# Optimization experiments

Measured on AMD Instinct MI355X. Metric: run time of the kernel, lower is better.

The kernel has to match this reference:

```python
import jax, jax.numpy as jnp
import numpy as np

B, T, DIM, H, HD = 2, 2048, 1024, 8, 128
ATTN_SCALE = 0.12  # attn_args.attn_scale (modded-nanogpt constant)
F32_EPS = float(np.finfo(np.float32).eps)  # F.rms_norm default eps


def ste_round(x):
    # straight-through round (round_grad_pt): identity gradient
    return x + jax.lax.stop_gradient(jnp.round(x) - x)


def quantized_linear(x, num_bits=8, eps=1e-5):
    num_steps = (2 ** num_bits - 1) // 2  # 127
    xnmin = jnp.minimum(jnp.min(x, -1, keepdims=True), -eps)
    xpmax = jnp.maximum(jnp.max(x, -1, keepdims=True), eps)
    xp = ste_round(x / xpmax * num_steps) / num_steps * xpmax
    xn = ste_round(x / xnmin * num_steps) / num_steps * xnmin
    return jnp.where(x >= 0, xp, xn)


def ternary_quantize_mean_special(w):
    # w: [3, hdim, dim]; per-leading-slice scale
    s = jnp.maximum(jnp.mean(jnp.mean(jnp.abs(w), -1, keepdims=True), -2, keepdims=True), 1e-5)
    return s * jnp.clip(ste_round(w / s), -1.0, 1.0)


def ternary_quantize(w):
    s = jnp.maximum(jnp.mean(jnp.abs(w)), 1e-5)
    return s * jnp.clip(ste_round(w / s), -1.0, 1.0)


def rmsnorm(x):
    return x * jax.lax.rsqrt(jnp.mean(x * x, -1, keepdims=True) + F32_EPS)


def rotary(x, cos, sin):
    # x: [B,T,H,HD]; cos,sin: [T, HD//2]
    x1, x2 = jnp.split(x, 2, axis=-1)
    c = cos[None, :, None, :]
    s = sin[None, :, None, :]
    return jnp.concatenate([x1 * c + x2 * s, -x1 * s + x2 * c], axis=-1)


def setup_inputs() -> dict:
    key = jax.random.key(0)
    ks = jax.random.split(key, 5)
    x = jax.random.normal(ks[0], (B, T, DIM), jnp.float32)
    ve = jax.random.normal(ks[1], (B, T, DIM), jnp.float32)
    sa_lambdas = jnp.array([0.5, 0.5], jnp.float32)
    inv_freq = 1.0 / (10000.0 ** (np.arange(0, HD, 2, dtype=np.float32) / HD))
    ang = np.arange(T, dtype=np.float32)[:, None] * inv_freq[None, :]
    cos = jnp.asarray(np.cos(ang), jnp.float32)
    sin = jnp.asarray(np.sin(ang), jnp.float32)
    bound = (3.0 ** 0.5) * 0.5 * DIM ** (-0.5)
    qkvo_w = jax.random.uniform(ks[2], (4, H * HD, DIM), jnp.float32, -bound, bound)
    gate_w = 0.1 * jax.random.normal(ks[3], (H, 12), jnp.float32)
    return {"x": x, "ve": ve, "sa_lambdas": sa_lambdas, "cos": cos, "sin": sin,
            "qkvo_w": qkvo_w, "gate_w": gate_w}


def reference(x, ve, sa_lambdas, cos, sin, qkvo_w, gate_w):
    # pre-activation int8 fake-quant (ENABLE_ATTN_PRE_ACT_QUANTIZATION)
    xq = quantized_linear(x, num_bits=8)
    # ternary-quantized QKV weights (ENABLE_ATTN_QUANTIZATION)
    w_qkv = ternary_quantize_mean_special(qkvo_w[:3]).reshape(3 * H * HD, DIM)
    qkv = jnp.einsum('btd,ed->bte', xq, w_qkv).reshape(B, T, 3 * H, HD)
    q, k, v = qkv[:, :, :H], qkv[:, :, H:2 * H], qkv[:, :, 2 * H:]
    q, k = rmsnorm(q), rmsnorm(k)
    q, k = rotary(q, cos, sin), rotary(k, cos, sin)
    v = sa_lambdas[0] * v + sa_lambdas[1] * ve.reshape(v.shape)
    # q/k int8 fake-quant (ENABLE_ATTN_ACT_QUANTIZATION)
    q = quantized_linear(q, num_bits=8)
    k = quantized_linear(k, num_bits=8)
    # causal SDPA with explicit scale
    scores = jnp.einsum('bqhd,bkhd->bhqk', q, k) * ATTN_SCALE
    mask = jnp.tril(jnp.ones((T, T), bool))
    scores = jnp.where(mask[None, None], scores, -jnp.inf)
    p = jax.nn.softmax(scores, axis=-1)
    y = jnp.einsum('bhqk,bkhd->bqhd', p, v)  # [B,T,H,HD]
    # sigmoid gate from first 12 features of (quantized) x
    gate = jax.nn.sigmoid(jnp.einsum('btf,hf->bth', xq[..., :12], gate_w))
    y = (y * gate[..., None]).reshape(B, T, H * HD)
    # ternary-quantized output projection (ENABLE_ATTN_PROJ_QUANTIZATION)
    w_o = ternary_quantize(qkvo_w[3])
    return jnp.einsum('bte,de->btd', y, w_o)
```

## Files before the change

kernel.cpp:

```cpp
#include <hip/hip_runtime.h>
#include <hip/hip_bf16.h>
#include <cstddef>
#include <cstdint>

#define B_    2
#define T_    2048
#define DIM_  1024
#define H_    8
#define HD_   128
#define BT_   (B_*T_)
#define E3_   (3*H_*HD_)
#define F32_EPS_ 1.1920929e-07f
#define QSC_  0.17312340490667562f

typedef __attribute__((ext_vector_type(8))) short bh8_t;
typedef __attribute__((ext_vector_type(4))) float f32x4_t;
typedef __attribute__((ext_vector_type(16))) float f32x16_t;
typedef __attribute__((ext_vector_type(4))) unsigned short us4_t;

__device__ inline unsigned short bf16r(float f) {
    unsigned u = __builtin_bit_cast(unsigned, f);
    u = (u + 0x7fffu + ((u >> 16) & 1u)) >> 16;
    return (unsigned short)u;
}
__device__ inline float b2f(unsigned short u) {
    return __builtin_bit_cast(float, (unsigned)u << 16);
}
__device__ inline unsigned cvtpk(float a, float b) {
    unsigned r;
    asm("v_cvt_pk_bf16_f32 %0, %1, %2" : "=v"(r) : "v"(a), "v"(b));
    return r;
}
__device__ inline void gl16(const unsigned short* g, unsigned short* l) {
    __builtin_amdgcn_global_load_lds((const __attribute__((address_space(1))) void*)g,
                                     (__attribute__((address_space(3))) void*)l, 16, 0, 0);
}

__global__ __launch_bounds__(256) void absmean1_kernel(const float* __restrict__ w, float* __restrict__ partial) {
    int blk = blockIdx.x;
    size_t off = (size_t)blk * 4096;
    __shared__ float red[256];
    int tid = threadIdx.x;
    float acc = 0.f;
    const float* p = w + off + tid*16;
    #pragma unroll
    for (int j = 0; j < 4; j++) {
        float4 v = *(const float4*)(p + j*4);
        acc += fabsf(v.x) + fabsf(v.y) + fabsf(v.z) + fabsf(v.w);
    }
    red[tid] = acc; __syncthreads();
    for (int s = 128; s > 0; s >>= 1) { if (tid < s) red[tid] += red[tid+s]; __syncthreads(); }
    if (tid == 0) partial[blk] = red[0];
}

__global__ __launch_bounds__(256) void absmean2_kernel(const float* __restrict__ partial, float* __restrict__ scales) {
    int m = blockIdx.x;
    __shared__ float red[256];
    int tid = threadIdx.x;
    red[tid] = partial[m*256 + tid]; __syncthreads();
    for (int s = 128; s > 0; s >>= 1) { if (tid < s) red[tid] += red[tid+s]; __syncthreads(); }
    if (tid == 0) scales[m] = fmaxf(red[0] / (float)(DIM_*DIM_), 1e-5f);
}

__global__ __launch_bounds__(256) void quant_w_kernel(const float* __restrict__ w, const float* __restrict__ scales,
                                                      unsigned short* __restrict__ wq) {
    int base = (blockIdx.x * 256 + threadIdx.x) * 8;
    float s = scales[base >> 20];
    float inv = 1.f / s;
    unsigned short out[8];
    float4 v0 = *(const float4*)(w + base);
    float4 v1 = *(const float4*)(w + base + 4);
    float t[8] = {v0.x, v0.y, v0.z, v0.w, v1.x, v1.y, v1.z, v1.w};
    #pragma unroll
    for (int j = 0; j < 8; j++) {
        float r = rintf(t[j] * inv);
        r = fminf(1.f, fmaxf(-1.f, r));
        out[j] = (r == 0.f) ? 0 : (r > 0.f ? 0x3F80 : 0xBF80);
    }
    *(int4*)(wq + base) = *(const int4*)out;
}

__global__ __launch_bounds__(256) void quant_x_gate_kernel(const float* __restrict__ x, const float* __restrict__ gw,
                                                           unsigned short* __restrict__ xqb, float* __restrict__ gate) {
    int row = blockIdx.x;
    const float* xr = x + (size_t)row * DIM_;
    unsigned short* qr = xqb + (size_t)row * DIM_;
    __shared__ float red[256];
    __shared__ float x12[12];
    int tid = threadIdx.x;
    float v[4];
    float mn = 1e30f, mx = -1e30f;
    #pragma unroll
    for (int i = 0; i < 4; i++) {
        v[i] = xr[i*256 + tid];
        mn = fminf(mn, v[i]); mx = fmaxf(mx, v[i]);
    }
    red[tid] = mn; __syncthreads();
    for (int s = 128; s > 0; s >>= 1) { if (tid < s) red[tid] = fminf(red[tid], red[tid+s]); __syncthreads(); }
    mn = red[0]; __syncthreads();
    red[tid] = mx; __syncthreads();
    for (int s = 128; s > 0; s >>= 1) { if (tid < s) red[tid] = fmaxf(red[tid], red[tid+s]); __syncthreads(); }
    mx = red[0]; __syncthreads();
    float p = fmaxf(mx, 1e-5f);
    float n = fminf(mn, -1e-5f);
    #pragma unroll
    for (int i = 0; i < 4; i++) {
        int gi = i*256 + tid;
        float xv = v[i];
        float sc = (xv >= 0.f) ? p : n;
        float q = rintf(xv / sc * 127.f) / 127.f * sc;
        qr[gi] = bf16r(q);
        if (gi < 12) x12[gi] = q;
    }
    __syncthreads();
    if (tid < H_) {
        float acc = 0.f;
        #pragma unroll
        for (int f = 0; f < 12; f++) acc += x12[f] * gw[tid*12 + f];
        gate[(size_t)row * H_ + tid] = 1.f / (1.f + expf(-acc));
    }
}

template<int MT, bool OBF>
__global__ __launch_bounds__(256) void gemm_bf16_kernel(const unsigned short* __restrict__ A,
                                                        const unsigned short* __restrict__ Bm,
                                                        const float* __restrict__ sw, int sbase,
                                                        void* __restrict__ Cv, int M, int N, int K) {
    __shared__ __align__(16) unsigned short As[MT*32*64];
    __shared__ __align__(16) unsigned short Bs[128*64];
    int bm = blockIdx.y * (MT*32), bn = blockIdx.x * 128;
    int tid = threadIdx.x;
    int w = tid >> 6, l = tid & 63;
    int wr = w >> 1, wc = w & 1;
    int lg = l >> 4, lq = l & 15;
    f32x4_t acc[MT][4];
    #pragma unroll
    for (int mt = 0; mt < MT; mt++)
        #pragma unroll
        for (int nt = 0; nt < 4; nt++) acc[mt][nt] = (f32x4_t)0.f;

    for (int k0 = 0; k0 < K; k0 += 64) {
        #pragma unroll
        for (int i = 0; i < MT; i++) {
            int ob = (i*4 + w) << 10;
            int o  = ob + (l << 4);
            int row = o >> 7;
            int lcn = ((o >> 4) & 7) ^ (row & 7);
            gl16(A + (size_t)(bm+row)*K + k0 + lcn*8, (unsigned short*)As + (ob >> 1));
        }
        #pragma unroll
        for (int i = 0; i < 4; i++) {
            int ob = (i*4 + w) << 10;
            int o  = ob + (l << 4);
            int row = o >> 7;
            int lcn = ((o >> 4) & 7) ^ (row & 7);
            gl16(Bm + (size_t)(bn+row)*K + k0 + lcn*8, (unsigned short*)Bs + (ob >> 1));
        }
        __syncthreads();
        #pragma unroll
        for (int kk = 0; kk < 2; kk++) {
            bh8_t af[MT], bf[4];
            #pragma unroll
            for (int mt = 0; mt < MT; mt++) {
                int r = wr*(MT*16) + mt*16 + lq;
                int j = kk*4 + lg;
                af[mt] = *(const bh8_t*)(As + r*64 + (((j ^ (r & 7)))<<3));
            }
            #pragma unroll
            for (int nt = 0; nt < 4; nt++) {
                int r = wc*64 + nt*16 + lq;
                int j = kk*4 + lg;
                bf[nt] = *(const bh8_t*)(Bs + r*64 + (((j ^ (r & 7)))<<3));
            }
            #pragma unroll
            for (int mt = 0; mt < MT; mt++)
                #pragma unroll
                for (int nt = 0; nt < 4; nt++)
                    acc[mt][nt] = __builtin_amdgcn_mfma_f32_16x16x32_bf16(af[mt], bf[nt], acc[mt][nt], 0, 0, 0);
        }
        __syncthreads();
    }
    #pragma unroll
    for (int nt = 0; nt < 4; nt++) {
        int col = bn + wc*64 + nt*16 + lq;
        float s = sw[sbase + (col >> 10)];
        #pragma unroll
        for (int mt = 0; mt < MT; mt++) {
            int row = bm + wr*(MT*16) + mt*16 + lg*4;
            #pragma unroll
            for (int r = 0; r < 4; r++) {
                if constexpr (OBF)
                    ((unsigned short*)Cv)[(size_t)(row + r)*N + col] = bf16r(acc[mt][nt][r] * s);
                else
                    ((float*)Cv)[(size_t)(row + r)*N + col] = acc[mt][nt][r] * s;
            }
        }
    }
}

__global__ __launch_bounds__(256) void qkv_post_kernel(const unsigned short* __restrict__ qkvb,
                                                       const float* __restrict__ ve,
                                                       const float* __restrict__ lam,
                                                       const float* __restrict__ cosb, const float* __restrict__ sinb,
                                                       unsigned short* __restrict__ Qb, unsigned short* __restrict__ Kb,
                                                       unsigned short* __restrict__ Vb) {
    int bt = blockIdx.x;
    int b = bt >> 11, t = bt & (T_ - 1);
    int w = threadIdx.x >> 6, l = threadIdx.x & 63;
    const unsigned short* base = qkvb + (size_t)bt * E3_;
    float l0 = lam[0], l1 = lam[1];
    #pragma unroll
    for (int i = 0; i < 2; i++) {
        int h = w*2 + i;
        const unsigned short* row = base + (16 + h)*HD_;
        const float* ver = ve + (size_t)bt*DIM_ + h*HD_;
        unsigned short* dst = Vb + ((size_t)(b*H_+h)*T_ + t)*HD_;
        dst[l]      = bf16r(l0*b2f(row[l])    + l1*ver[l]);
        dst[l + 64] = bf16r(l0*b2f(row[l+64]) + l1*ver[l+64]);
    }
    float cc = cosb[(size_t)t*64 + l], ss = sinb[(size_t)t*64 + l];
    #pragma unroll
    for (int i = 0; i < 4; i++) {
        int part = w*4 + i;
        const unsigned short* row = base + part*HD_;
        float x1 = b2f(row[l]), x2 = b2f(row[l+64]);
        float ssq = x1*x1 + x2*x2;
        #pragma unroll
        for (int off = 1; off < 64; off <<= 1) ssq += __shfl_xor(ssq, off);
        float rms = 1.0f / sqrtf(ssq / 128.0f + F32_EPS_);
        x1 *= rms; x2 *= rms;
        float o1 = x1*cc + x2*ss;
        float o2 = -x1*ss + x2*cc;
        float mn = fminf(o1, o2), mx = fmaxf(o1, o2);
        #pragma unroll
        for (int off = 1; off < 64; off <<= 1) {
            mn = fminf(mn, __shfl_xor(mn, off));
            mx = fmaxf(mx, __shfl_xor(mx, off));
        }
        float p = fmaxf(mx, 1e-5f);
        float n = fminf(mn, -1e-5f);
        float s1 = (o1 >= 0.f) ? p : n;
        float s2 = (o2 >= 0.f) ? p : n;
        float q1 = rintf(o1 / s1 * 127.f) / 127.f * s1;
        float q2 = rintf(o2 / s2 * 127.f) / 127.f * s2;
        if (part < 8) {
            unsigned short* dst = Qb + ((size_t)(b*H_+part)*T_ + t)*HD_;
            dst[l] = bf16r(QSC_ * q1); dst[l + 64] = bf16r(QSC_ * q2);
        } else {
            unsigned short* dst = Kb + ((size_t)(b*H_+part-8)*T_ + t)*HD_;
            dst[l] = bf16r(q1); dst[l + 64] = bf16r(q2);
        }
    }
}

__global__ __launch_bounds__(256) void transpose_v_kernel(const unsigned short* __restrict__ Vb,
                                                          unsigned short* __restrict__ VT) {
    int tt = blockIdx.x;
    int dt = blockIdx.y;
    int bh = blockIdx.z;
    __shared__ unsigned short L[64][80];
    int tid = threadIdx.x;
    #pragma unroll
    for (int i = 0; i < 2; i++) {
        int c = tid + i*256;
        int r = c >> 3, dc = c & 7;
        int4 v = *(const int4*)(Vb + ((size_t)bh*T_ + tt*64 + r)*HD_ + dt*64 + dc*8);
        *(int4*)(&L[r][dc*8]) = v;
    }
    __syncthreads();
    #pragma unroll
    for (int i = 0; i < 2; i++) {
        int c = tid + i*256;
        int r = c >> 3, tc = c & 7;
        unsigned short tmp[8];
        #pragma unroll
        for (int jj = 0; jj < 8; jj++) tmp[jj] = L[tc*8+jj][r];
        *(int4*)(VT + ((size_t)bh*HD_ + dt*64 + r)*T_ + tt*64 + tc*8) = *(const int4*)tmp;
    }
}

__global__ __launch_bounds__(256) void attn_kernel(const unsigned short* __restrict__ Qb,
                                                   const unsigned short* __restrict__ Kb,
                                                   const unsigned short* __restrict__ VT,
                                                   const float* __restrict__ gate,
                                                   unsigned short* __restrict__ Yb,
                                                   unsigned short* __restrict__ Opart,
                                                   float* __restrict__ MLg) {
    __shared__ __align__(16) unsigned char SMEM[65536];
    int rid = 1279 - (int)blockIdx.x;
    int bh = rid & 15;
    int idx = rid >> 4;
    int qt, c, nc;
    if (idx < 8)       { qt = idx;                 c = 0;           nc = 1; }
    else if (idx < 24) { int t = idx - 8;  qt = 8  + (t >> 1);  c = t & 1;      nc = 2; }
    else if (idx < 48) { int t = idx - 24; qt = 16 + t / 3;     c = t - 3*(t/3); nc = 3; }
    else               { int t = idx - 48; qt = 24 + (t >> 2);  c = t & 3;      nc = 4; }
    int pslot = (idx - 8)*16 + bh;
    int b = bh >> 3, h = bh & 7;
    int tid = threadIdx.x;
    int w = tid >> 6, l = tid & 63;
    int qsub = w >> 1, qq = w & 1;
    int hh = l >> 5, l5 = l & 31;
    int qrow = qsub*32 + l5;
    int qg = qt*64 + qrow;

    const unsigned short* Kbase = Kb + (size_t)bh*T_*HD_;
    const unsigned short* Vbase = VT + (size_t)bh*HD_*T_;
    const unsigned short* Qg = Qb + ((size_t)bh*T_ + (size_t)qt*64) * HD_;

    bh8_t qf[8];
    #pragma unroll
    for (int ks = 0; ks < 8; ks++)
        qf[ks] = *(const bh8_t*)(Qg + (size_t)qrow*HD_ + ks*16 + hh*8);

    int j0c  = c*8;
    int jend = (qt + 1 < j0c + 8) ? (qt + 1) : (j0c + 8);
    int ncr  = jend - j0c;

    f32x16_t o0 = (f32x16_t)0.f, o1 = (f32x16_t)0.f, o2 = (f32x16_t)0.f, o3 = (f32x16_t)0.f;
    float mrun = -1e20f, lrun = 0.f;

#define STAGE(BI, J) { \
    unsigned short* kb_ = (unsigned short*)(SMEM + (BI)*16384); \
    unsigned short* vb_ = (unsigned short*)(SMEM + 32768 + (BI)*16384); \
    _Pragma("unroll") \
    for (int i_ = 0; i_ < 4; i_++) { \
        int ob_ = (i_*4 + w) << 10; \
        int o_  = ob_ + (l << 4); \
        int rk_ = o_ >> 8; \
        int lk_ = ((o_ >> 4) & 15) ^ (rk_ & 15); \
        gl16(Kbase + (size_t)((J)*64 + rk_)*HD_ + lk_*8, kb_ + (ob_ >> 1)); \
        int rv_ = o_ >> 7; \
        int lv_ = ((o_ >> 4) & 7) ^ (rv_ & 7); \
        gl16(Vbase + (size_t)rv_*T_ + (J)*64 + lv_*8, vb_ + (ob_ >> 1)); \
    } }

    STAGE(0, j0c);
    for (int jj = 0; jj < ncr; jj++) {
        int j = j0c + jj;
        if (jj + 1 < ncr) {
            STAGE((jj+1) & 1, j+1);
            asm volatile("s_waitcnt vmcnt(8)" ::: "memory");
        } else {
            asm volatile("s_waitcnt vmcnt(0)" ::: "memory");
        }
        __builtin_amdgcn_s_barrier();
        asm volatile("" ::: "memory");
        const unsigned short* kb = (const unsigned short*)(SMEM + (jj&1)*16384);
        const unsigned short* vb = (const unsigned short*)(SMEM + 32768 + (jj&1)*16384);
        int kvb = j*64 + qq*32;
        if (kvb <= qt*64 + qsub*32 + 31) {
            f32x16_t s = (f32x16_t)0.f;
            int krow = qq*32 + l5;
            __builtin_amdgcn_s_setprio(1);
            #pragma unroll
            for (int ks = 0; ks < 8; ks++) {
                int cch = (ks*2 + hh) ^ (krow & 15);
                bh8_t kf = *(const bh8_t*)(kb + krow*128 + cch*8);
                s = __builtin_amdgcn_mfma_f32_32x32x16_bf16(kf, qf[ks], s, 0, 0, 0);
            }
            __builtin_amdgcn_s_setprio(0);
            if (kvb + 31 > qt*64 + qsub*32) {
                #pragma unroll
                for (int r = 0; r < 16; r++) {
                    int key = kvb + (r & 3) + 8*(r >> 2) + 4*hh;
                    if (key > qg) s[r] = -1e30f;
                }
            }
            float t8[8], t4[4];
            #pragma unroll
            for (int r = 0; r < 8; r++) t8[r] = fmaxf(s[2*r], s[2*r+1]);
            #pragma unroll
            for (int r = 0; r < 4; r++) t4[r] = fmaxf(t8[2*r], t8[2*r+1]);
            float tm = fmaxf(fmaxf(t4[0], t4[1]), fmaxf(t4[2], t4[3]));
            tm = fmaxf(tm, __shfl_xor(tm, 32));
            if (!__all(tm - mrun <= 8.f)) {
                float mnew = fmaxf(mrun, tm);
                float scf = __builtin_amdgcn_exp2f(mrun - mnew);
                lrun *= scf;
                o0 *= scf; o1 *= scf; o2 *= scf; o3 *= scf;
                mrun = mnew;
            }
            float p[16];
            #pragma unroll
            for (int r = 0; r < 16; r++) p[r] = __builtin_amdgcn_exp2f(s[r] - mrun);
            #pragma unroll
            for (int r = 0; r < 8; r++) t8[r] = p[2*r] + p[2*r+1];
            #pragma unroll
            for (int r = 0; r < 4; r++) t4[r] = t8[2*r] + t8[2*r+1];
            float ls = (t4[0] + t4[1]) + (t4[2] + t4[3]);
            ls += __shfl_xor(ls, 32);
            lrun += ls;
            unsigned u0 = cvtpk(p[0], p[1]),   u1 = cvtpk(p[2], p[3]);
            unsigned u2 = cvtpk(p[4], p[5]),   u3 = cvtpk(p[6], p[7]);
            unsigned u4 = cvtpk(p[8], p[9]),   u5 = cvtpk(p[10], p[11]);
            unsigned u6 = cvtpk(p[12], p[13]), u7 = cvtpk(p[14], p[15]);
            unsigned x0 = (unsigned)__shfl_xor((int)u0, 32), x1 = (unsigned)__shfl_xor((int)u1, 32);
            unsigned x2 = (unsigned)__shfl_xor((int)u2, 32), x3 = (unsigned)__shfl_xor((int)u3, 32);
            unsigned x4 = (unsigned)__shfl_xor((int)u4, 32), x5 = (unsigned)__shfl_xor((int)u5, 32);
            unsigned x6 = (unsigned)__shfl_xor((int)u6, 32), x7 = (unsigned)__shfl_xor((int)u7, 32);
            union { bh8_t v; unsigned uu[4]; } B0, B1;
            B0.uu[0] = hh ? x2 : u0;  B0.uu[1] = hh ? x3 : u1;
            B0.uu[2] = hh ? u2 : x0;  B0.uu[3] = hh ? u3 : x1;
            B1.uu[0] = hh ? x6 : u4;  B1.uu[1] = hh ? x7 : u5;
            B1.uu[2] = hh ? u6 : x4;  B1.uu[3] = hh ? u7 : x5;
            __builtin_amdgcn_s_setprio(1);
#define PV_STEP(DT, OACC) { \
    int vrow = DT*32 + l5; \
    bh8_t vf0 = *(const bh8_t*)(vb + vrow*64 + (((qq*4 + hh) ^ (vrow & 7))<<3)); \
    OACC = __builtin_amdgcn_mfma_f32_32x32x16_bf16(vf0, B0.v, OACC, 0, 0, 0); \
    bh8_t vf1 = *(const bh8_t*)(vb + vrow*64 + (((qq*4 + 2 + hh) ^ (vrow & 7))<<3)); \
    OACC = __builtin_amdgcn_mfma_f32_32x32x16_bf16(vf1, B1.v, OACC, 0, 0, 0); }
            PV_STEP(0, o0) PV_STEP(1, o1) PV_STEP(2, o2) PV_STEP(3, o3)
#undef PV_STEP
            __builtin_amdgcn_s_setprio(0);
        }
        asm volatile("s_waitcnt lgkmcnt(0)" ::: "memory");
        __builtin_amdgcn_s_barrier();
        asm volatile("" ::: "memory");
    }

    f32x16_t oA[4] = {o0, o1, o2, o3};
    float* OB = (float*)SMEM;
    float* ML = (float*)(SMEM + 32768);
    unsigned short* YS = (unsigned short*)(SMEM + 33280);
    if (qq != 0) {
        float* obuf = OB + (size_t)qsub * 4096;
        #pragma unroll
        for (int dt = 0; dt < 4; dt++)
            #pragma unroll
            for (int g = 0; g < 4; g++) {
                f32x4_t v4;
                #pragma unroll
                for (int e = 0; e < 4; e++) v4[e] = oA[dt][g*4+e];
                int ch = (dt*4 + g) ^ (l & 7);
                *(f32x4_t*)(obuf + l*64 + ch*4) = v4;
            }
        if (hh == 0) {
            ML[(qsub*32 + l5)*2]     = mrun;
            ML[(qsub*32 + l5)*2 + 1] = lrun;
        }
    }
    __syncthreads();
    if (qq == 0) {
        float mb = ML[(qsub*32 + l5)*2];
        float lb = ML[(qsub*32 + l5)*2 + 1];
        float mN = fmaxf(mrun, mb);
        float fa = __builtin_amdgcn_exp2f(mrun - mN), fb = __builtin_amdgcn_exp2f(mb - mN);
        const float* obuf = OB + (size_t)qsub * 4096;
        #pragma unroll
        for (int dt = 0; dt < 4; dt++)
            #pragma unroll
            for (int g = 0; g < 4; g++) {
                int ch = (dt*4 + g) ^ (l & 7);
                f32x4_t v4 = *(const f32x4_t*)(obuf + l*64 + ch*4);
                #pragma unroll
                for (int e = 0; e < 4; e++)
                    oA[dt][g*4+e] = oA[dt][g*4+e]*fa + v4[e]*fb;
            }
        lrun = lrun*fa + lb*fb;
        mrun = mN;
        float inv;
        if (nc == 1) {
            float gv = gate[((size_t)b*T_ + (size_t)qg)*H_ + h];
            inv = gv / lrun;
        } else {
            inv = 1.f / lrun;
            if (hh == 0) {
                MLg[(size_t)pslot*128 + qrow*2]     = mrun;
                MLg[(size_t)pslot*128 + qrow*2 + 1] = lrun;
            }
        }
        #pragma unroll
        for (int dt = 0; dt < 4; dt++)
            #pragma unroll
            for (int g = 0; g < 4; g++) {
                unsigned short pk4[4];
                #pragma unroll
                for (int e = 0; e < 4; e++) pk4[e] = bf16r(oA[dt][g*4+e] * inv);
                int ch = (dt*4 + g) ^ (qrow & 7);
                *(us4_t*)(YS + (size_t)qrow*128 + ch*8 + hh*4) = *(const us4_t*)pk4;
            }
    }
    __syncthreads();
    if (nc == 1) {
        #pragma unroll
        for (int i = 0; i < 4; i++) {
            int idx2 = tid + i*256;
            int r = idx2 >> 4, scn = idx2 & 15;
            int lcn = scn ^ (r & 7);
            int4 v = *(const int4*)(YS + (size_t)r*128 + scn*8);
            *(int4*)(Yb + (size_t)(b*T_ + qt*64 + r)*DIM_ + h*HD_ + lcn*8) = v;
        }
    } else {
        unsigned short* od = Opart + (size_t)pslot*8192;
        #pragma unroll
        for (int i = 0; i < 4; i++) {
            int idx2 = tid + i*256;
            int r = idx2 >> 4, scn = idx2 & 15;
            int lcn = scn ^ (r & 7);
            int4 v = *(const int4*)(YS + (size_t)r*128 + scn*8);
            *(int4*)(od + (size_t)r*128 + lcn*8) = v;
        }
    }
#undef STAGE
}

__global__ __launch_bounds__(256) void attn_merge_kernel(const unsigned short* __restrict__ Opart,
                                                         const float* __restrict__ MLg,
                                                         const float* __restrict__ gate,
                                                         unsigned short* __restrict__ Yb) {
    int mblk = blockIdx.x;
    int bh = mblk & 15, ti = mblk >> 4;
    int qt = 8 + ti;
    int nc, base;
    if (qt < 16)      { nc = 2; base = 8  + (qt - 8)*2;  }
    else if (qt < 24) { nc = 3; base = 24 + (qt - 16)*3; }
    else              { nc = 4; base = 48 + (qt - 24)*4; }
    int b = bh >> 3, h = bh & 7;
    int row = threadIdx.x >> 2;
    int d0  = (threadIdx.x & 3) * 32;

    float mc[4], lc[4];
    float m = -1e30f;
    #pragma unroll
    for (int cc = 0; cc < 4; cc++) {
        if (cc < nc) {
            int ps = (base + cc - 8)*16 + bh;
            mc[cc] = MLg[(size_t)ps*128 + row*2];
            lc[cc] = MLg[(size_t)ps*128 + row*2 + 1];
            m = fmaxf(m, mc[cc]);
        }
    }
    float num[32];
    #pragma unroll
    for (int e = 0; e < 32; e++) num[e] = 0.f;
    float den = 0.f;
    #pragma unroll
    for (int cc = 0; cc < 4; cc++) {
        if (cc < nc) {
            int ps = (base + cc - 8)*16 + bh;
            float wgt = lc[cc] * __builtin_amdgcn_exp2f(mc[cc] - m);
            den += wgt;
            const unsigned short* op = Opart + (size_t)ps*8192 + row*128 + d0;
            #pragma unroll
            for (int e8 = 0; e8 < 4; e8++) {
                union { int4 v; unsigned short q[8]; } u;
                u.v = *(const int4*)(op + e8*8);
                #pragma unroll
                for (int k = 0; k < 8; k++) num[e8*8 + k] += wgt * b2f(u.q[k]);
            }
        }
    }
    float gv = gate[((size_t)b*T_ + qt*64 + row)*H_ + h];
    float s = gv / den;
    unsigned short* yd = Yb + (size_t)(b*T_ + qt*64 + row)*DIM_ + h*HD_ + d0;
    #pragma unroll
    for (int e8 = 0; e8 < 4; e8++) {
        unsigned short pk8[8];
        #pragma unroll
        for (int k = 0; k < 8; k++) pk8[k] = bf16r(num[e8*8 + k] * s);
        *(int4*)(yd + e8*8) = *(const int4*)pk8;
    }
}

extern "C" void kernel_launch(void* const* d_in, const int* in_sizes, int n_in,
                              void* d_out, int out_size, void* d_ws, size_t ws_size,
                              hipStream_t stream) {
    const float* x    = (const float*)d_in[0];
    const float* ve   = (const float*)d_in[1];
    const float* lam  = (const float*)d_in[2];
    const float* cosb = (const float*)d_in[3];
    const float* sinb = (const float*)d_in[4];
    const float* qkvo = (const float*)d_in[5];
    const float* gw   = (const float*)d_in[6];

    char* ws = (char*)d_ws;
    float* scales  = (float*)ws;
    float* partial = scales + 16;
    unsigned short* WQb  = (unsigned short*)(ws + (1<<13));
    unsigned short* XQb  = WQb + (size_t)4*DIM_*DIM_;
    unsigned short* QKVb = XQb + (size_t)BT_*DIM_;
    float* GT = (float*)(QKVb + (size_t)BT_*E3_);
    unsigned short* Qb = (unsigned short*)(GT + (size_t)BT_*H_);
    unsigned short* Kb = Qb + (size_t)B_*H_*T_*HD_;
    unsigned short* VT = Kb + (size_t)B_*H_*T_*HD_;
    unsigned short* Vb = VT + (size_t)B_*H_*T_*HD_;
    unsigned short* Yb = XQb;
    unsigned short* Opart = QKVb;
    float* MLg = (float*)(Opart + (size_t)1152*8192);

    absmean1_kernel<<<1024, 256, 0, stream>>>(qkvo, partial);
    absmean2_kernel<<<4, 256, 0, stream>>>(partial, scales);
    quant_w_kernel<<<(4*DIM_*DIM_)/(256*8), 256, 0, stream>>>(qkvo, scales, WQb);
    quant_x_gate_kernel<<<BT_, 256, 0, stream>>>(x, gw, XQb, GT);
    gemm_bf16_kernel<4, true><<<dim3(E3_/128, BT_/128), 256, 0, stream>>>(XQb, WQb, scales, 0, QKVb, BT_, E3_, DIM_);
    qkv_post_kernel<<<BT_, 256, 0, stream>>>(QKVb, ve, lam, cosb, sinb, Qb, Kb, Vb);
    transpose_v_kernel<<<dim3(T_/64, HD_/64, B_*H_), 256, 0, stream>>>(Vb, VT);
    attn_kernel<<<1280, 256, 0, stream>>>(Qb, Kb, VT, GT, Yb, Opart, MLg);
    attn_merge_kernel<<<384, 256, 0, stream>>>(Opart, MLg, GT, Yb);
    gemm_bf16_kernel<2, false><<<dim3(DIM_/128, BT_/64), 256, 0, stream>>>(Yb, WQb + (size_t)3*DIM_*DIM_, scales, 3,
                                                                           (float*)d_out, BT_, DIM_, DIM_);
}
```

Measured before the change: 151.1 us.

## Shrink attention blocks to two waves with 32-key tiles, dropping intra-block merge

```diff
diff --git a/kernel.cpp b/kernel.cpp
--- a/kernel.cpp
+++ b/kernel.cpp
@@ -279,30 +279,32 @@
     }
 }
 
-__global__ __launch_bounds__(256) void attn_kernel(const unsigned short* __restrict__ Qb,
+__global__ __launch_bounds__(128) void attn_kernel(const unsigned short* __restrict__ Qb,
                                                    const unsigned short* __restrict__ Kb,
                                                    const unsigned short* __restrict__ VT,
                                                    const float* __restrict__ gate,
                                                    unsigned short* __restrict__ Yb,
                                                    unsigned short* __restrict__ Opart,
                                                    float* __restrict__ MLg) {
-    __shared__ __align__(16) unsigned char SMEM[65536];
-    int rid = 1279 - (int)blockIdx.x;
-    int bh = rid & 15;
-    int idx = rid >> 4;
+    __shared__ __align__(16) unsigned char SMEM[32768];
+    int bh  = blockIdx.x & 15;
+    int idx = blockIdx.x >> 4;
     int qt, c, nc;
-    if (idx < 8)       { qt = idx;                 c = 0;           nc = 1; }
-    else if (idx < 24) { int t = idx - 8;  qt = 8  + (t >> 1);  c = t & 1;      nc = 2; }
-    else if (idx < 48) { int t = idx - 24; qt = 16 + t / 3;     c = t - 3*(t/3); nc = 3; }
-    else               { int t = idx - 48; qt = 24 + (t >> 2);  c = t & 3;      nc = 4; }
-    int pslot = (idx - 8)*16 + bh;
+    if (idx < 8)       { qt = idx;                           c = 0;            nc = 1; }
+    else if (idx < 24) { int t = idx - 8;  qt = 8  + (t>>1); c = t & 1;        nc = 2; }
+    else if (idx < 48) { int t = idx - 24; qt = 16 + t/3;    c = t - 3*(t/3);  nc = 3; }
+    else               { int t = idx - 48; qt = 24 + (t>>2); c = t & 3;        nc = 4; }
     int b = bh >> 3, h = bh & 7;
     int tid = threadIdx.x;
     int w = tid >> 6, l = tid & 63;
-    int qsub = w >> 1, qq = w & 1;
     int hh = l >> 5, l5 = l & 31;
-    int qrow = qsub*32 + l5;
+    int qrow = w*32 + l5;
     int qg = qt*64 + qrow;
+    int qwbase = qt*64 + w*32;
+
+    int nrt  = 2*qt + 2;
+    int j0   = c*16;
+    int jend = (nrt < j0 + 16) ? nrt : (j0 + 16);
 
     const unsigned short* Kbase = Kb + (size_t)bh*T_*HD_;
     const unsigned short* Vbase = VT + (size_t)bh*HD_*T_;
@@ -313,63 +315,59 @@
     for (int ks = 0; ks < 8; ks++)
         qf[ks] = *(const bh8_t*)(Qg + (size_t)qrow*HD_ + ks*16 + hh*8);
 
-    int j0c  = c*8;
-    int jend = (qt + 1 < j0c + 8) ? (qt + 1) : (j0c + 8);
-    int ncr  = jend - j0c;
-
     f32x16_t o0 = (f32x16_t)0.f, o1 = (f32x16_t)0.f, o2 = (f32x16_t)0.f, o3 = (f32x16_t)0.f;
     float mrun = -1e20f, lrun = 0.f;
 
 #define STAGE(BI, J) { \
     unsigned short* kb_ = (unsigned short*)(SMEM + (BI)*16384); \
-    unsigned short* vb_ = (unsigned short*)(SMEM + 32768 + (BI)*16384); \
+    unsigned short* vb_ = (unsigned short*)(SMEM + (BI)*16384 + 8192); \
     _Pragma("unroll") \
     for (int i_ = 0; i_ < 4; i_++) { \
-        int ob_ = (i_*4 + w) << 10; \
+        int ob_ = (i_*2 + w) << 10; \
         int o_  = ob_ + (l << 4); \
         int rk_ = o_ >> 8; \
         int lk_ = ((o_ >> 4) & 15) ^ (rk_ & 15); \
-        gl16(Kbase + (size_t)((J)*64 + rk_)*HD_ + lk_*8, kb_ + (ob_ >> 1)); \
-        int rv_ = o_ >> 7; \
-        int lv_ = ((o_ >> 4) & 7) ^ (rv_ & 7); \
-        gl16(Vbase + (size_t)rv_*T_ + (J)*64 + lv_*8, vb_ + (ob_ >> 1)); \
+        gl16(Kbase + (size_t)((J)*32 + rk_)*HD_ + lk_*8, kb_ + (ob_ >> 1)); \
+        int rv_ = o_ >> 6; \
+        int lv_ = ((o_ >> 4) & 3) ^ (rv_ & 3); \
+        gl16(Vbase + (size_t)rv_*T_ + (J)*32 + lv_*8, vb_ + (ob_ >> 1)); \
     } }
 
-    STAGE(0, j0c);
-    for (int jj = 0; jj < ncr; jj++) {
-        int j = j0c + jj;
-        if (jj + 1 < ncr) {
-            STAGE((jj+1) & 1, j+1);
+    STAGE(0, j0);
+    for (int j = j0; j < jend; j++) {
+        int cur = (j - j0) & 1;
+        if (j + 1 < jend) {
+            STAGE(cur ^ 1, j+1);
             asm volatile("s_waitcnt vmcnt(8)" ::: "memory");
         } else {
             asm volatile("s_waitcnt vmcnt(0)" ::: "memory");
         }
         __builtin_amdgcn_s_barrier();
         asm volatile("" ::: "memory");
-        const unsigned short* kb = (const unsigned short*)(SMEM + (jj&1)*16384);
-        const unsigned short* vb = (const unsigned short*)(SMEM + 32768 + (jj&1)*16384);
-        int kvb = j*64 + qq*32;
-        if (kvb <= qt*64 + qsub*32 + 31) {
-            f32x16_t s = (f32x16_t)0.f;
-            int krow = qq*32 + l5;
+        const unsigned short* kb = (const unsigned short*)(SMEM + cur*16384);
+        const unsigned short* vb = (const unsigned short*)(SMEM + cur*16384 + 8192);
+        int kvb = j*32;
+        if (kvb <= qwbase + 31) {
+            f32x16_t sA = (f32x16_t)0.f;
+            int krow = l5;
             __builtin_amdgcn_s_setprio(1);
             #pragma unroll
             for (int ks = 0; ks < 8; ks++) {
                 int cch = (ks*2 + hh) ^ (krow & 15);
                 bh8_t kf = *(const bh8_t*)(kb + krow*128 + cch*8);
-                s = __builtin_amdgcn_mfma_f32_32x32x16_bf16(kf, qf[ks], s, 0, 0, 0);
+                sA = __builtin_amdgcn_mfma_f32_32x32x16_bf16(kf, qf[ks], sA, 0, 0, 0);
             }
             __builtin_amdgcn_s_setprio(0);
-            if (kvb + 31 > qt*64 + qsub*32) {
+            if (kvb + 31 > qwbase) {
                 #pragma unroll
                 for (int r = 0; r < 16; r++) {
                     int key = kvb + (r & 3) + 8*(r >> 2) + 4*hh;
-                    if (key > qg) s[r] = -1e30f;
+                    if (key > qg) sA[r] = -1e30f;
                 }
             }
             float t8[8], t4[4];
             #pragma unroll
-            for (int r = 0; r < 8; r++) t8[r] = fmaxf(s[2*r], s[2*r+1]);
+            for (int r = 0; r < 8; r++) t8[r] = fmaxf(sA[2*r], sA[2*r+1]);
             #pragma unroll
             for (int r = 0; r < 4; r++) t4[r] = fmaxf(t8[2*r], t8[2*r+1]);
             float tm = fmaxf(fmaxf(t4[0], t4[1]), fmaxf(t4[2], t4[3]));
@@ -381,20 +379,20 @@
                 o0 *= scf; o1 *= scf; o2 *= scf; o3 *= scf;
                 mrun = mnew;
             }
-            float p[16];
-            #pragma unroll
-            for (int r = 0; r < 16; r++) p[r] = __builtin_amdgcn_exp2f(s[r] - mrun);
-            #pragma unroll
-            for (int r = 0; r < 8; r++) t8[r] = p[2*r] + p[2*r+1];
+            float pp[16];
+            #pragma unroll
+            for (int r = 0; r < 16; r++) pp[r] = __builtin_amdgcn_exp2f(sA[r] - mrun);
+            #pragma unroll
+            for (int r = 0; r < 8; r++) t8[r] = pp[2*r] + pp[2*r+1];
             #pragma unroll
             for (int r = 0; r < 4; r++) t4[r] = t8[2*r] + t8[2*r+1];
             float ls = (t4[0] + t4[1]) + (t4[2] + t4[3]);
             ls += __shfl_xor(ls, 32);
             lrun += ls;
-            unsigned u0 = cvtpk(p[0], p[1]),   u1 = cvtpk(p[2], p[3]);
-            unsigned u2 = cvtpk(p[4], p[5]),   u3 = cvtpk(p[6], p[7]);
-            unsigned u4 = cvtpk(p[8], p[9]),   u5 = cvtpk(p[10], p[11]);
-            unsigned u6 = cvtpk(p[12], p[13]), u7 = cvtpk(p[14], p[15]);
+            unsigned u0 = cvtpk(pp[0], pp[1]),   u1 = cvtpk(pp[2], pp[3]);
+            unsigned u2 = cvtpk(pp[4], pp[5]),   u3 = cvtpk(pp[6], pp[7]);
+            unsigned u4 = cvtpk(pp[8], pp[9]),   u5 = cvtpk(pp[10], pp[11]);
+            unsigned u6 = cvtpk(pp[12], pp[13]), u7 = cvtpk(pp[14], pp[15]);
             unsigned x0 = (unsigned)__shfl_xor((int)u0, 32), x1 = (unsigned)__shfl_xor((int)u1, 32);
             unsigned x2 = (unsigned)__shfl_xor((int)u2, 32), x3 = (unsigned)__shfl_xor((int)u3, 32);
             unsigned x4 = (unsigned)__shfl_xor((int)u4, 32), x5 = (unsigned)__shfl_xor((int)u5, 32);
@@ -407,9 +405,9 @@
             __builtin_amdgcn_s_setprio(1);
 #define PV_STEP(DT, OACC) { \
     int vrow = DT*32 + l5; \
-    bh8_t vf0 = *(const bh8_t*)(vb + vrow*64 + (((qq*4 + hh) ^ (vrow & 7))<<3)); \
+    bh8_t vf0 = *(const bh8_t*)(vb + vrow*32 + (((hh) ^ (vrow & 3))<<3)); \
     OACC = __builtin_amdgcn_mfma_f32_32x32x16_bf16(vf0, B0.v, OACC, 0, 0, 0); \
-    bh8_t vf1 = *(const bh8_t*)(vb + vrow*64 + (((qq*4 + 2 + hh) ^ (vrow & 7))<<3)); \
+    bh8_t vf1 = *(const bh8_t*)(vb + vrow*32 + (((2 + hh) ^ (vrow & 3))<<3)); \
     OACC = __builtin_amdgcn_mfma_f32_32x32x16_bf16(vf1, B1.v, OACC, 0, 0, 0); }
             PV_STEP(0, o0) PV_STEP(1, o1) PV_STEP(2, o2) PV_STEP(3, o3)
 #undef PV_STEP
@@ -421,85 +419,46 @@
     }
 
     f32x16_t oA[4] = {o0, o1, o2, o3};
-    float* OB = (float*)SMEM;
-    float* ML = (float*)(SMEM + 32768);
-    unsigned short* YS = (unsigned short*)(SMEM + 33280);
-    if (qq != 0) {
-        float* obuf = OB + (size_t)qsub * 4096;
-        #pragma unroll
-        for (int dt = 0; dt < 4; dt++)
-            #pragma unroll
-            for (int g = 0; g < 4; g++) {
-                f32x4_t v4;
-                #pragma unroll
-                for (int e = 0; e < 4; e++) v4[e] = oA[dt][g*4+e];
-                int ch = (dt*4 + g) ^ (l & 7);
-                *(f32x4_t*)(obuf + l*64 + ch*4) = v4;
-            }
+    unsigned short* ys = (unsigned short*)(SMEM + w*8192);
+    float inv;
+    int pslot = idx*16 + bh;
+    if (nc == 1) {
+        float gv = gate[((size_t)b*T_ + (size_t)qg)*H_ + h];
+        inv = gv / lrun;
+    } else {
+        inv = (lrun > 0.f) ? (1.f / lrun) : 0.f;
         if (hh == 0) {
-            ML[(qsub*32 + l5)*2]     = mrun;
-            ML[(qsub*32 + l5)*2 + 1] = lrun;
-        }
-    }
-    __syncthreads();
-    if (qq == 0) {
-        float mb = ML[(qsub*32 + l5)*2];
-        float lb = ML[(qsub*32 + l5)*2 + 1];
-        float mN = fmaxf(mrun, mb);
-        float fa = __builtin_amdgcn_exp2f(mrun - mN), fb = __builtin_amdgcn_exp2f(mb - mN);
-        const float* obuf = OB + (size_t)qsub * 4096;
-        #pragma unroll
-        for (int dt = 0; dt < 4; dt++)
-            #pragma unroll
-            for (int g = 0; g < 4; g++) {
-                int ch = (dt*4 + g) ^ (l & 7);
-                f32x4_t v4 = *(const f32x4_t*)(obuf + l*64 + ch*4);
-                #pragma unroll
-                for (int e = 0; e < 4; e++)
-                    oA[dt][g*4+e] = oA[dt][g*4+e]*fa + v4[e]*fb;
-            }
-        lrun = lrun*fa + lb*fb;
-        mrun = mN;
-        float inv;
-        if (nc == 1) {
-            float gv = gate[((size_t)b*T_ + (size_t)qg)*H_ + h];
-            inv = gv / lrun;
-        } else {
-            inv = 1.f / lrun;
-            if (hh == 0) {
-                MLg[(size_t)pslot*128 + qrow*2]     = mrun;
-                MLg[(size_t)pslot*128 + qrow*2 + 1] = lrun;
-            }
-        }
-        #pragma unroll
-        for (int dt = 0; dt < 4; dt++)
-            #pragma unroll
-            for (int g = 0; g < 4; g++) {
-                unsigned short pk4[4];
-                #pragma unroll
-                for (int e = 0; e < 4; e++) pk4[e] = bf16r(oA[dt][g*4+e] * inv);
-                int ch = (dt*4 + g) ^ (qrow & 7);
-                *(us4_t*)(YS + (size_t)qrow*128 + ch*8 + hh*4) = *(const us4_t*)pk4;
-            }
-    }
-    __syncthreads();
+            MLg[(size_t)pslot*128 + qrow*2]     = mrun;
+            MLg[(size_t)pslot*128 + qrow*2 + 1] = lrun;
+        }
+    }
+    #pragma unroll
+    for (int dt = 0; dt < 4; dt++)
+        #pragma unroll
+        for (int gg = 0; gg < 4; gg++) {
+            unsigned short pk4[4];
+            #pragma unroll
+            for (int e = 0; e < 4; e++) pk4[e] = bf16r(oA[dt][gg*4+e] * inv);
+            int ch = (dt*4 + gg) ^ (l5 & 7);
+            *(us4_t*)(ys + (size_t)l5*128 + ch*8 + hh*4) = *(const us4_t*)pk4;
+        }
     if (nc == 1) {
         #pragma unroll
-        for (int i = 0; i < 4; i++) {
-            int idx2 = tid + i*256;
+        for (int i = 0; i < 8; i++) {
+            int idx2 = l + i*64;
             int r = idx2 >> 4, scn = idx2 & 15;
             int lcn = scn ^ (r & 7);
-            int4 v = *(const int4*)(YS + (size_t)r*128 + scn*8);
-            *(int4*)(Yb + (size_t)(b*T_ + qt*64 + r)*DIM_ + h*HD_ + lcn*8) = v;
+            int4 v = *(const int4*)(ys + (size_t)r*128 + scn*8);
+            *(int4*)(Yb + (size_t)(b*T_ + qt*64 + w*32 + r)*DIM_ + h*HD_ + lcn*8) = v;
         }
     } else {
-        unsigned short* od = Opart + (size_t)pslot*8192;
-        #pragma unroll
-        for (int i = 0; i < 4; i++) {
-            int idx2 = tid + i*256;
+        unsigned short* od = Opart + (size_t)pslot*8192 + (size_t)w*32*128;
+        #pragma unroll
+        for (int i = 0; i < 8; i++) {
+            int idx2 = l + i*64;
             int r = idx2 >> 4, scn = idx2 & 15;
             int lcn = scn ^ (r & 7);
-            int4 v = *(const int4*)(YS + (size_t)r*128 + scn*8);
+            int4 v = *(const int4*)(ys + (size_t)r*128 + scn*8);
             *(int4*)(od + (size_t)r*128 + lcn*8) = v;
         }
     }
@@ -511,8 +470,8 @@
                                                          const float* __restrict__ gate,
                                                          unsigned short* __restrict__ Yb) {
     int mblk = blockIdx.x;
-    int bh = mblk & 15, ti = mblk >> 4;
-    int qt = 8 + ti;
+    int bh = mblk & 15;
+    int qt = 8 + (mblk >> 4);
     int nc, base;
     if (qt < 16)      { nc = 2; base = 8  + (qt - 8)*2;  }
     else if (qt < 24) { nc = 3; base = 24 + (qt - 16)*3; }
@@ -526,7 +485,7 @@
     #pragma unroll
     for (int cc = 0; cc < 4; cc++) {
         if (cc < nc) {
-            int ps = (base + cc - 8)*16 + bh;
+            int ps = (base + cc)*16 + bh;
             mc[cc] = MLg[(size_t)ps*128 + row*2];
             lc[cc] = MLg[(size_t)ps*128 + row*2 + 1];
             m = fmaxf(m, mc[cc]);
@@ -539,7 +498,7 @@
     #pragma unroll
     for (int cc = 0; cc < 4; cc++) {
         if (cc < nc) {
-            int ps = (base + cc - 8)*16 + bh;
+            int ps = (base + cc)*16 + bh;
             float wgt = lc[cc] * __builtin_amdgcn_exp2f(mc[cc] - m);
             den += wgt;
             const unsigned short* op = Opart + (size_t)ps*8192 + row*128 + d0;
@@ -586,9 +545,9 @@
     unsigned short* Kb = Qb + (size_t)B_*H_*T_*HD_;
     unsigned short* VT = Kb + (size_t)B_*H_*T_*HD_;
     unsigned short* Vb = VT + (size_t)B_*H_*T_*HD_;
-    unsigned short* Yb = XQb;
-    unsigned short* Opart = QKVb;
-    float* MLg = (float*)(Opart + (size_t)1152*8192);
+    unsigned short* Opart = Vb + (size_t)B_*H_*T_*HD_;
+    float* MLg = (float*)(Opart + (size_t)1280*8192);
+    unsigned short* Yb = QKVb;
 
     absmean1_kernel<<<1024, 256, 0, stream>>>(qkvo, partial);
     absmean2_kernel<<<4, 256, 0, stream>>>(partial, scales);
@@ -597,7 +556,7 @@
     gemm_bf16_kernel<4, true><<<dim3(E3_/128, BT_/128), 256, 0, stream>>>(XQb, WQb, scales, 0, QKVb, BT_, E3_, DIM_);
     qkv_post_kernel<<<BT_, 256, 0, stream>>>(QKVb, ve, lam, cosb, sinb, Qb, Kb, Vb);
     transpose_v_kernel<<<dim3(T_/64, HD_/64, B_*H_), 256, 0, stream>>>(Vb, VT);
-    attn_kernel<<<1280, 256, 0, stream>>>(Qb, Kb, VT, GT, Yb, Opart, MLg);
+    attn_kernel<<<1280, 128, 0, stream>>>(Qb, Kb, VT, GT, Yb, Opart, MLg);
     attn_merge_kernel<<<384, 256, 0, stream>>>(Opart, MLg, GT, Yb);
     gemm_bf16_kernel<2, false><<<dim3(DIM_/128, BT_/64), 256, 0, stream>>>(Yb, WQb + (size_t)3*DIM_*DIM_, scales, 3,
                                                                            (float*)d_out, BT_, DIM_, DIM_);
```

Measured after the change: 155.2 us. +2.8%, slower.
